# Optimization experiments

Measured on AMD Instinct MI355X. Metric: run time of the kernel, lower is better.

Reference implementation:

```python
import jax, jax.numpy as jnp
import numpy as np

N = 50000        # num_nodes
E = 800000       # num_edges (avg degree 16)
K = 3            # Chebyshev order
F_IN = 144       # 144 * in_channels
F_OUT = 144      # 144 * out_channels


def setup_inputs() -> dict:
    key = jax.random.key(0)
    k1, k2, k3, k4, k5 = jax.random.split(key, 5)
    x = jax.random.normal(k1, (N, F_IN), dtype=jnp.float32)
    edge_index = jax.random.randint(k2, (2, E), 0, N, dtype=jnp.int32)
    edge_weight = jax.random.uniform(k3, (E,), dtype=jnp.float32)
    weight = jax.random.normal(k4, (K, F_IN, F_OUT), dtype=jnp.float32) * 0.02
    bias = jax.random.normal(k5, (F_OUT,), dtype=jnp.float32) * 0.02
    return {"x": x, "edge_index": edge_index, "edge_weight": edge_weight,
            "weight": weight, "bias": bias}


def reference(x, edge_index, edge_weight, weight, bias):
    row, col = edge_index[0], edge_index[1]
    # remove_self_loops: mask out edges with row == col (fixed-shape equivalent)
    mask = (row != col).astype(x.dtype)
    w = edge_weight * mask
    # degree over remaining edges, deg^-0.5 with inf -> 0
    deg = jax.ops.segment_sum(mask, row, num_segments=N)
    dinv = jnp.where(deg > 0, deg ** -0.5, jnp.zeros_like(deg))
    lap = -dinv[row] * w * dinv[col]  # [E]

    def spmm(v):  # out[i] = sum_{e: row_e = i} lap_e * v[col_e]
        return jax.ops.segment_sum(lap[:, None] * v[col], row, num_segments=N)

    Tx0 = x
    out = Tx0 @ weight[0]
    Tx1 = spmm(Tx0)
    out = out + Tx1 @ weight[1]
    for k in range(2, weight.shape[0]):
        Tx2 = 2.0 * spmm(Tx1) - Tx0
        out = out + Tx2 @ weight[k]
        Tx0, Tx1 = Tx1, Tx2
    return out + bias
```

## Files before the change

### kernel.cpp

```cpp
#include <hip/hip_runtime.h>
#include <hip/hip_bf16.h>

#define NN 50000
#define EE 800000
#define FF 144
#define CVTBLK 1758
#define ECHK 2048
#define NBE 391
#define NBKT_REAL 391
#define NBUCKET 392
#define WGRID 284
#define HM (NBUCKET * NBE)
#define SCANBLK 599

typedef __hip_bfloat16 bf16;
typedef __attribute__((ext_vector_type(8))) short short8;
typedef __attribute__((ext_vector_type(4))) float floatx4;
typedef __attribute__((ext_vector_type(2))) float float2v;

__device__ inline float blo(unsigned x) { return __uint_as_float(x << 16); }
__device__ inline float bhi(unsigned x) { return __uint_as_float(x & 0xffff0000u); }

__device__ inline void dec4fma(float* a, float l, unsigned d) {
    float2v p0 = __builtin_amdgcn_cvt_pk_f32_fp8((int)d, false);
    float2v p1 = __builtin_amdgcn_cvt_pk_f32_fp8((int)d, true);
    a[0] = fmaf(l, p0.x, a[0]);
    a[1] = fmaf(l, p0.y, a[1]);
    a[2] = fmaf(l, p1.x, a[2]);
    a[3] = fmaf(l, p1.y, a[3]);
}
__device__ inline void fma16q(float* a, float l, uint4 u) {
    dec4fma(a + 0, l, u.x);
    dec4fma(a + 4, l, u.y);
    dec4fma(a + 8, l, u.z);
    dec4fma(a + 12, l, u.w);
}
__device__ inline unsigned enc4(float a, float b, float c, float d) {
    int w = __builtin_amdgcn_cvt_pk_fp8_f32(a, b, 0, false);
    w = __builtin_amdgcn_cvt_pk_fp8_f32(c, d, w, true);
    return (unsigned)w;
}


__global__ void detect_k(const int* __restrict__ ei, int* __restrict__ flag) {
    __shared__ int nz;
    if (threadIdx.x == 0) nz = 0;
    __syncthreads();
    if (ei[2 * threadIdx.x + 1] != 0) atomicAdd(&nz, 1);
    __syncthreads();
    if (threadIdx.x == 0) *flag = (nz == 0) ? 1 : 0;
}

__device__ inline void load_edge(const int* ei, int e, int flag, int& r, int& c) {
    if (flag) { r = ei[2 * e]; c = ei[2 * EE + 2 * e]; }
    else      { r = ei[e];     c = ei[EE + e]; }
}


__global__ void fusedA_k(const float* __restrict__ x, bf16* __restrict__ xb,
                         unsigned char* __restrict__ xq,
                         const int* __restrict__ ei, const float* __restrict__ ew,
                         unsigned long long* __restrict__ items, int* __restrict__ hist,
                         const float* __restrict__ wt, short* __restrict__ wtb,
                         const int* __restrict__ flagp) {
    __shared__ int lh[NBUCKET];
    int b = blockIdx.x;
    int tid = threadIdx.x;
    if (b < CVTBLK) {
        int t = b * 256 + tid;
        if (t >= NN * FF / 16) return;
        const float4* xp = (const float4*)x + t * 4;
        float4 v0 = xp[0], v1 = xp[1], v2 = xp[2], v3 = xp[3];
        float f[16] = {v0.x, v0.y, v0.z, v0.w, v1.x, v1.y, v1.z, v1.w,
                       v2.x, v2.y, v2.z, v2.w, v3.x, v3.y, v3.z, v3.w};
        unsigned short hs[16];
        #pragma unroll
        for (int j = 0; j < 16; ++j) {
            bf16 bb = (bf16)f[j];
            hs[j] = *(unsigned short*)&bb;
        }
        uint4* xbq = (uint4*)xb + t * 2;
        xbq[0] = ((uint4*)hs)[0];
        xbq[1] = ((uint4*)hs)[1];
        uint4 q;
        q.x = enc4(f[0], f[1], f[2], f[3]);
        q.y = enc4(f[4], f[5], f[6], f[7]);
        q.z = enc4(f[8], f[9], f[10], f[11]);
        q.w = enc4(f[12], f[13], f[14], f[15]);
        ((uint4*)xq)[t] = q;
    } else if (b < CVTBLK + NBE) {
        int bb = b - CVTBLK;
        for (int j = tid; j < NBUCKET; j += 256) lh[j] = 0;
        __syncthreads();
        int flag = *flagp;
        int eb = bb * ECHK;
        #pragma unroll
        for (int k = 0; k < ECHK / 256; ++k) {
            int e = eb + k * 256 + tid;
            if (e < EE) {
                int r, c; load_edge(ei, e, flag, r, c);
                unsigned key = (r == c) ? 0xFFFFu : (unsigned)r;
                float w = ew[e];
                items[e] = ((unsigned long long)((key << 16) | (unsigned)c) << 32)
                           | (unsigned long long)__float_as_uint(w);
                atomicAdd(&lh[min(key >> 7, (unsigned)NBKT_REAL)], 1);
            }
        }
        __syncthreads();
        for (int j = tid; j < NBUCKET; j += 256) hist[j * NBE + bb] = lh[j];
    } else {
        int t = (b - CVTBLK - NBE) * 256 + tid;
        if (t >= 3 * FF * 168) return;
        int ph = t / (FF * 168);
        int rem = t - ph * FF * 168;
        int o = rem / 168;
        int i = rem - o * 168;
        short v = 0;
        if (i < FF) {
            bf16 bv = (bf16)wt[ph * FF * FF + i * FF + o];
            v = *(const short*)&bv;
        }
        wtb[t] = v;
    }
}


__global__ void scanA1_k(int* __restrict__ hist, int* __restrict__ bsumA) {
    __shared__ int wsum[4], woff[4];
    int b = blockIdx.x, tid = threadIdx.x;
    int wv = tid >> 6, ln = tid & 63;
    int i = b * 256 + tid;
    int v = (i < HM) ? hist[i] : 0;
    int xs = v;
    #pragma unroll
    for (int off = 1; off < 64; off <<= 1) {
        int t = __shfl_up(xs, off, 64);
        if (ln >= off) xs += t;
    }
    if (ln == 63) wsum[wv] = xs;
    __syncthreads();
    if (tid == 0) {
        int s = 0;
        #pragma unroll
        for (int j = 0; j < 4; ++j) { woff[j] = s; s += wsum[j]; }
        bsumA[b] = s;
    }
    __syncthreads();
    if (i < HM) hist[i] = woff[wv] + (xs - v);
}

__global__ __launch_bounds__(1024) void scanA2_k(int* __restrict__ bsumA) {
    __shared__ int wsum[16], woff[16];
    int tid = threadIdx.x, wv = tid >> 6, ln = tid & 63;
    int v = (tid < SCANBLK) ? bsumA[tid] : 0;
    int xs = v;
    #pragma unroll
    for (int off = 1; off < 64; off <<= 1) {
        int t = __shfl_up(xs, off, 64);
        if (ln >= off) xs += t;
    }
    if (ln == 63) wsum[wv] = xs;
    __syncthreads();
    if (tid == 0) {
        int s = 0;
        #pragma unroll
        for (int j = 0; j < 16; ++j) { woff[j] = s; s += wsum[j]; }
    }
    __syncthreads();
    if (tid < SCANBLK) bsumA[tid] = woff[wv] + (xs - v);
}

__device__ inline int hbase(const int* hist, const int* bsumA, int f) {
    return hist[f] + bsumA[f >> 8];
}


__global__ void pscat_k(const unsigned long long* __restrict__ items,
                        const int* __restrict__ hist, const int* __restrict__ bsumA,
                        unsigned long long* __restrict__ sorted) {
    __shared__ int lbase[NBUCKET];
    int b = blockIdx.x, tid = threadIdx.x;
    for (int j = tid; j < NBUCKET; j += 256) {
        int f = j * NBE + b;
        lbase[j] = hbase(hist, bsumA, f);
    }
    __syncthreads();
    int eb = b * ECHK;
    #pragma unroll
    for (int k = 0; k < ECHK / 256; ++k) {
        int e = eb + k * 256 + tid;
        if (e < EE) {
            unsigned long long it = items[e];
            unsigned key = (unsigned)(it >> 48);
            int bk = (int)min(key >> 7, (unsigned)NBKT_REAL);
            int slot = atomicAdd(&lbase[bk], 1);
            sorted[slot] = it;
        }
    }
}


__global__ void fine1_k(const unsigned long long* __restrict__ sorted,
                        const int* __restrict__ hist, const int* __restrict__ bsumA,
                        int* __restrict__ rowptr, float* __restrict__ dinv) {
    __shared__ int lh[128];
    __shared__ int wtot;
    int b = blockIdx.x, tid = threadIdx.x;
    if (tid < 128) lh[tid] = 0;
    int s = hbase(hist, bsumA, b * NBE);
    int e = hbase(hist, bsumA, (b + 1) * NBE);
    __syncthreads();
    for (int p = s + tid; p < e; p += 256)
        atomicAdd(&lh[(int)(unsigned)(sorted[p] >> 48) - b * 128], 1);
    __syncthreads();
    int ln = tid & 63;
    int v = (tid < 128) ? lh[tid] : 0;
    int xs = v;
    #pragma unroll
    for (int off = 1; off < 64; off <<= 1) {
        int t = __shfl_up(xs, off, 64);
        if (ln >= off) xs += t;
    }
    if (tid == 63) wtot = xs;
    __syncthreads();
    int excl = xs - v + ((tid >= 64 && tid < 128) ? wtot : 0);
    int gr = b * 128 + tid;
    if (tid < 128 && gr < NN) {
        rowptr[gr] = s + excl;
        dinv[gr] = v > 0 ? rsqrtf((float)v) : 0.f;
    }
    if (b == NBKT_REAL - 1 && tid == 0) rowptr[NN] = e;
}


__global__ void fine2_k(const unsigned long long* __restrict__ sorted,
                        const int* __restrict__ hist, const int* __restrict__ bsumA,
                        const int* __restrict__ rowptr, const float* __restrict__ dinv,
                        unsigned* __restrict__ pairs) {
    __shared__ int lrp[128];
    __shared__ float ldv[128];
    int b = blockIdx.x, tid = threadIdx.x;
    int gr = b * 128 + tid;
    if (tid < 128) {
        lrp[tid] = (gr < NN) ? rowptr[gr] : 0;
        ldv[tid] = (gr < NN) ? dinv[gr] : 0.f;
    }
    int s = hbase(hist, bsumA, b * NBE);
    int e = hbase(hist, bsumA, (b + 1) * NBE);
    __syncthreads();
    for (int p = s + tid; p < e; p += 256) {
        unsigned long long it = sorted[p];
        int lr = (int)(unsigned)(it >> 48) - b * 128;
        unsigned c = (unsigned)(it >> 32) & 0xFFFFu;
        float w = __uint_as_float((unsigned)it);
        float lap = -ldv[lr] * dinv[c] * w;
        int slot = atomicAdd(&lrp[lr], 1);
        bf16 lb = (bf16)lap;
        pairs[slot] = c | ((unsigned)*(unsigned short*)&lb << 16);
    }
}


template <int MODE>
__global__ void spmm_k(const unsigned char* __restrict__ vq, const bf16* __restrict__ x0,
                       const int* __restrict__ rowptr, const unsigned* __restrict__ pairs,
                       bf16* __restrict__ y, unsigned char* __restrict__ yq) {
    int t = blockIdx.x * 256 + threadIdx.x;
    if (t >= NN * 9) return;
    int i = t / 9;
    int fo = (t - i * 9) * 16;
    const unsigned char* vp = vq + fo;

    float a[16];
    #pragma unroll
    for (int j = 0; j < 16; ++j) a[j] = 0.f;

    int s = rowptr[i], e = rowptr[i + 1];
    int p = s;
    for (; p + 1 < e; p += 2) {
        unsigned pr0 = pairs[p], pr1 = pairs[p + 1];
        uint4 u0 = *(const uint4*)(vp + (pr0 & 0xffffu) * FF);
        uint4 u1 = *(const uint4*)(vp + (pr1 & 0xffffu) * FF);
        fma16q(a, bhi(pr0), u0);
        fma16q(a, bhi(pr1), u1);
    }
    if (p < e) {
        unsigned pr = pairs[p];
        uint4 u = *(const uint4*)(vp + (pr & 0xffffu) * FF);
        fma16q(a, bhi(pr), u);
    }

    if (MODE == 1) {
        const uint4* xp = (const uint4*)((const unsigned short*)x0 + i * FF + fo);
        uint4 u0 = xp[0], u1 = xp[1];
        a[0]  = 2.f * a[0]  - blo(u0.x);  a[1]  = 2.f * a[1]  - bhi(u0.x);
        a[2]  = 2.f * a[2]  - blo(u0.y);  a[3]  = 2.f * a[3]  - bhi(u0.y);
        a[4]  = 2.f * a[4]  - blo(u0.z);  a[5]  = 2.f * a[5]  - bhi(u0.z);
        a[6]  = 2.f * a[6]  - blo(u0.w);  a[7]  = 2.f * a[7]  - bhi(u0.w);
        a[8]  = 2.f * a[8]  - blo(u1.x);  a[9]  = 2.f * a[9]  - bhi(u1.x);
        a[10] = 2.f * a[10] - blo(u1.y);  a[11] = 2.f * a[11] - bhi(u1.y);
        a[12] = 2.f * a[12] - blo(u1.z);  a[13] = 2.f * a[13] - bhi(u1.z);
        a[14] = 2.f * a[14] - blo(u1.w);  a[15] = 2.f * a[15] - bhi(u1.w);
    }

    unsigned short hs[16];
    #pragma unroll
    for (int j = 0; j < 16; ++j) {
        bf16 b = (bf16)a[j];
        hs[j] = *(unsigned short*)&b;
    }
    uint4* yp = (uint4*)((unsigned short*)y + i * FF + fo);
    yp[0] = ((uint4*)hs)[0];
    yp[1] = ((uint4*)hs)[1];

    if (MODE == 0) {
        uint4 q;
        q.x = enc4(a[0], a[1], a[2], a[3]);
        q.y = enc4(a[4], a[5], a[6], a[7]);
        q.z = enc4(a[8], a[9], a[10], a[11]);
        q.w = enc4(a[12], a[13], a[14], a[15]);
        *(uint4*)(yq + i * FF + fo) = q;
    }
}


__global__ __launch_bounds__(1024)
void gemm_fused(const bf16* __restrict__ A0, const bf16* __restrict__ A1,
                const bf16* __restrict__ A2, const short* __restrict__ wtb,
                const float* __restrict__ bias, float* __restrict__ out) {
    __shared__ __align__(16) short Wt[3 * 144 * 168];
    int tid = threadIdx.x;

    {
        const uint4* Wg = (const uint4*)wtb;
        uint4* Wl = (uint4*)Wt;
        #pragma unroll
        for (int q = 0; q < 9; ++q) {
            int idx = q * 1024 + tid;
            if (idx < 9072) Wl[idx] = Wg[idx];
        }
    }
    __syncthreads();

    int wv = tid >> 6, ln = tid & 63;
    int m16 = ln & 15, quad = ln >> 4;
    int tile = wv * 256 + blockIdx.x;
    if (tile * 16 >= NN) return;
    int rowBase = tile * 16;
    int row = rowBase + m16;

    const bf16* const srcs[3] = {A0, A1, A2};
    const short8 zero8 = {0, 0, 0, 0, 0, 0, 0, 0};

    floatx4 acc[9];
    #pragma unroll
    for (int q = 0; q < 9; ++q) acc[q] = (floatx4){0.f, 0.f, 0.f, 0.f};

    #pragma unroll
    for (int ph = 0; ph < 3; ++ph) {
        const bf16* A = srcs[ph];
        short8 a[5];
        #pragma unroll
        for (int kt = 0; kt < 5; ++kt) {
            int k0 = kt * 32 + quad * 8;
            if (k0 < FF)
                a[kt] = *(const short8*)((const short*)A + row * FF + k0);
            else
                a[kt] = zero8;
        }

        const short* Wp = Wt + ph * 144 * 168;
        #pragma unroll
        for (int nt = 0; nt < 9; ++nt) {
            #pragma unroll
            for (int kt = 0; kt < 5; ++kt) {
                short8 b = *(const short8*)&Wp[(nt * 16 + m16) * 168 + kt * 32 + quad * 8];
                acc[nt] = __builtin_amdgcn_mfma_f32_16x16x32_bf16(a[kt], b, acc[nt], 0, 0, 0);
            }
        }
    }

    int rowc = rowBase + quad * 4;
    #pragma unroll
    for (int nt = 0; nt < 9; ++nt) {
        int col = nt * 16 + m16;
        float bs = bias[col];
        #pragma unroll
        for (int r = 0; r < 4; ++r) {
            int rr = rowc + r;
            out[rr * FF + col] = acc[nt][r] + bs;
        }
    }
}


extern "C" void kernel_launch(void* const* d_in, const int* in_sizes, int n_in,
                              void* d_out, int out_size, void* d_ws, size_t ws_size,
                              hipStream_t stream) {
    int ix = -1, iei = -1, iew = -1, iwt = -1, ib = -1;
    for (int i = 0; i < n_in; ++i) {
        switch (in_sizes[i]) {
            case NN * FF:      if (ix  < 0) ix  = i; break;
            case 2 * EE:       if (iei < 0) iei = i; break;
            case EE:           if (iew < 0) iew = i; break;
            case 3 * FF * FF:  if (iwt < 0) iwt = i; break;
            case FF:           if (ib  < 0) ib  = i; break;
        }
    }
    if (ix < 0 || iei < 0 || iew < 0 || iwt < 0 || ib < 0) {
        ix = 0; iei = 1; iew = 2; iwt = 3; ib = 4;
    }
    const float* x    = (const float*)d_in[ix];
    const int*   ei   = (const int*)d_in[iei];
    const float* ew   = (const float*)d_in[iew];
    const float* wt   = (const float*)d_in[iwt];
    const float* bias = (const float*)d_in[ib];
    float* out = (float*)d_out;

    char* p = (char*)d_ws;
    unsigned long long* items  = (unsigned long long*)(p + 0);
    unsigned long long* sorted = (unsigned long long*)(p + 6400000);
    int*      hist   = (int*)(p + 12800000);
    int*      bsumA  = (int*)(p + 13500000);
    int*      rowptr = (int*)(p + 13600000);
    float*    dinv   = (float*)(p + 13900000);
    unsigned* pairs  = (unsigned*)(p + 14200000);
    int*      eflag  = (int*)(p + 17400000);
    short*    wtb    = (short*)(p + 17500000);
    bf16*     tx1    = (bf16*)(p + 17700000);
    bf16*     tx2    = (bf16*)(p + 32100000);
    unsigned char* xq   = (unsigned char*)(p + 46500000);
    unsigned char* tx1q = (unsigned char*)(p + 53700000);
    bf16*     xb     = (bf16*)(p + 60900000);

    if (ws_size < 75300000) return;

    int spGrid = (NN * 9 + 255) / 256;

    detect_k<<<1, 256, 0, stream>>>(ei, eflag);
    fusedA_k<<<CVTBLK + NBE + WGRID, 256, 0, stream>>>(x, xb, xq, ei, ew, items, hist,
                                                       wt, wtb, eflag);
    scanA1_k<<<SCANBLK, 256, 0, stream>>>(hist, bsumA);
    scanA2_k<<<1, 1024, 0, stream>>>(bsumA);
    pscat_k<<<NBE, 256, 0, stream>>>(items, hist, bsumA, sorted);
    fine1_k<<<NBKT_REAL, 256, 0, stream>>>(sorted, hist, bsumA, rowptr, dinv);
    fine2_k<<<NBKT_REAL, 256, 0, stream>>>(sorted, hist, bsumA, rowptr, dinv, pairs);

    spmm_k<0><<<spGrid, 256, 0, stream>>>(xq, xb, rowptr, pairs, tx1, tx1q);
    spmm_k<1><<<spGrid, 256, 0, stream>>>(tx1q, xb, rowptr, pairs, tx2, (unsigned char*)0);
    gemm_fused<<<256, 1024, 0, stream>>>(xb, tx1, tx2, wtb, bias, out);
}
```

Measured before the change: 189.0 us.

## Fold Chebyshev recurrence into weights, merge layout detection, enlarge edge chunks

```diff
diff --git a/kernel.cpp b/kernel.cpp
--- a/kernel.cpp
+++ b/kernel.cpp
@@ -5,13 +5,13 @@
 #define EE 800000
 #define FF 144
 #define CVTBLK 1758
-#define ECHK 2048
-#define NBE 391
+#define ECHK 8192
+#define NBE 98
 #define NBKT_REAL 391
 #define NBUCKET 392
 #define WGRID 284
 #define HM (NBUCKET * NBE)
-#define SCANBLK 599
+#define SCANBLK 151
 
 typedef __hip_bfloat16 bf16;
 typedef __attribute__((ext_vector_type(8))) short short8;
@@ -41,16 +41,6 @@
     return (unsigned)w;
 }
 
-
-__global__ void detect_k(const int* __restrict__ ei, int* __restrict__ flag) {
-    __shared__ int nz;
-    if (threadIdx.x == 0) nz = 0;
-    __syncthreads();
-    if (ei[2 * threadIdx.x + 1] != 0) atomicAdd(&nz, 1);
-    __syncthreads();
-    if (threadIdx.x == 0) *flag = (nz == 0) ? 1 : 0;
-}
-
 __device__ inline void load_edge(const int* ei, int e, int flag, int& r, int& c) {
     if (flag) { r = ei[2 * e]; c = ei[2 * EE + 2 * e]; }
     else      { r = ei[e];     c = ei[EE + e]; }
@@ -61,9 +51,9 @@
                          unsigned char* __restrict__ xq,
                          const int* __restrict__ ei, const float* __restrict__ ew,
                          unsigned long long* __restrict__ items, int* __restrict__ hist,
-                         const float* __restrict__ wt, short* __restrict__ wtb,
-                         const int* __restrict__ flagp) {
+                         const float* __restrict__ wt, short* __restrict__ wtb) {
     __shared__ int lh[NBUCKET];
+    __shared__ int nzf;
     int b = blockIdx.x;
     int tid = threadIdx.x;
     if (b < CVTBLK) {
@@ -90,19 +80,25 @@
         ((uint4*)xq)[t] = q;
     } else if (b < CVTBLK + NBE) {
         int bb = b - CVTBLK;
+        if (tid == 0) nzf = 0;
         for (int j = tid; j < NBUCKET; j += 256) lh[j] = 0;
         __syncthreads();
-        int flag = *flagp;
         int eb = bb * ECHK;
-        #pragma unroll
+        unsigned acc = 0;
+        for (int k = 0; k < ECHK / 256; ++k) {
+            int e = eb + k * 256 + tid;
+            if (e < EE) acc |= (unsigned)ei[2 * e + 1];
+        }
+        if (acc) nzf = 1;
+        __syncthreads();
+        int flag = (nzf == 0) ? 1 : 0;
         for (int k = 0; k < ECHK / 256; ++k) {
             int e = eb + k * 256 + tid;
             if (e < EE) {
                 int r, c; load_edge(ei, e, flag, r, c);
                 unsigned key = (r == c) ? 0xFFFFu : (unsigned)r;
-                float w = ew[e];
                 items[e] = ((unsigned long long)((key << 16) | (unsigned)c) << 32)
-                           | (unsigned long long)__float_as_uint(w);
+                           | (unsigned long long)__float_as_uint(ew[e]);
                 atomicAdd(&lh[min(key >> 7, (unsigned)NBKT_REAL)], 1);
             }
         }
@@ -117,7 +113,11 @@
         int i = rem - o * 168;
         short v = 0;
         if (i < FF) {
-            bf16 bv = (bf16)wt[ph * FF * FF + i * FF + o];
+            float fv;
+            if (ph == 0)      fv = wt[i * FF + o] - wt[2 * FF * FF + i * FF + o];
+            else if (ph == 1) fv = wt[FF * FF + i * FF + o];
+            else              fv = 2.0f * wt[2 * FF * FF + i * FF + o];
+            bf16 bv = (bf16)fv;
             v = *(const short*)&bv;
         }
         wtb[t] = v;
@@ -149,8 +149,8 @@
     if (i < HM) hist[i] = woff[wv] + (xs - v);
 }
 
-__global__ __launch_bounds__(1024) void scanA2_k(int* __restrict__ bsumA) {
-    __shared__ int wsum[16], woff[16];
+__global__ void scanA2_k(int* __restrict__ bsumA) {
+    __shared__ int wsum[4], woff[4];
     int tid = threadIdx.x, wv = tid >> 6, ln = tid & 63;
     int v = (tid < SCANBLK) ? bsumA[tid] : 0;
     int xs = v;
@@ -164,7 +164,7 @@
     if (tid == 0) {
         int s = 0;
         #pragma unroll
-        for (int j = 0; j < 16; ++j) { woff[j] = s; s += wsum[j]; }
+        for (int j = 0; j < 4; ++j) { woff[j] = s; s += wsum[j]; }
     }
     __syncthreads();
     if (tid < SCANBLK) bsumA[tid] = woff[wv] + (xs - v);
@@ -186,7 +186,6 @@
     }
     __syncthreads();
     int eb = b * ECHK;
-    #pragma unroll
     for (int k = 0; k < ECHK / 256; ++k) {
         int e = eb + k * 256 + tid;
         if (e < EE) {
@@ -261,8 +260,8 @@
 }
 
 
-template <int MODE>
-__global__ void spmm_k(const unsigned char* __restrict__ vq, const bf16* __restrict__ x0,
+template <int WRITEQ>
+__global__ void spmm_k(const unsigned char* __restrict__ vq,
                        const int* __restrict__ rowptr, const unsigned* __restrict__ pairs,
                        bf16* __restrict__ y, unsigned char* __restrict__ yq) {
     int t = blockIdx.x * 256 + threadIdx.x;
@@ -290,19 +289,6 @@
         fma16q(a, bhi(pr), u);
     }
 
-    if (MODE == 1) {
-        const uint4* xp = (const uint4*)((const unsigned short*)x0 + i * FF + fo);
-        uint4 u0 = xp[0], u1 = xp[1];
-        a[0]  = 2.f * a[0]  - blo(u0.x);  a[1]  = 2.f * a[1]  - bhi(u0.x);
-        a[2]  = 2.f * a[2]  - blo(u0.y);  a[3]  = 2.f * a[3]  - bhi(u0.y);
-        a[4]  = 2.f * a[4]  - blo(u0.z);  a[5]  = 2.f * a[5]  - bhi(u0.z);
-        a[6]  = 2.f * a[6]  - blo(u0.w);  a[7]  = 2.f * a[7]  - bhi(u0.w);
-        a[8]  = 2.f * a[8]  - blo(u1.x);  a[9]  = 2.f * a[9]  - bhi(u1.x);
-        a[10] = 2.f * a[10] - blo(u1.y);  a[11] = 2.f * a[11] - bhi(u1.y);
-        a[12] = 2.f * a[12] - blo(u1.z);  a[13] = 2.f * a[13] - bhi(u1.z);
-        a[14] = 2.f * a[14] - blo(u1.w);  a[15] = 2.f * a[15] - bhi(u1.w);
-    }
-
     unsigned short hs[16];
     #pragma unroll
     for (int j = 0; j < 16; ++j) {
@@ -313,7 +299,7 @@
     yp[0] = ((uint4*)hs)[0];
     yp[1] = ((uint4*)hs)[1];
 
-    if (MODE == 0) {
+    if (WRITEQ) {
         uint4 q;
         q.x = enc4(a[0], a[1], a[2], a[3]);
         q.y = enc4(a[4], a[5], a[6], a[7]);
@@ -425,7 +411,6 @@
     int*      rowptr = (int*)(p + 13600000);
     float*    dinv   = (float*)(p + 13900000);
     unsigned* pairs  = (unsigned*)(p + 14200000);
-    int*      eflag  = (int*)(p + 17400000);
     short*    wtb    = (short*)(p + 17500000);
     bf16*     tx1    = (bf16*)(p + 17700000);
     bf16*     tx2    = (bf16*)(p + 32100000);
@@ -437,16 +422,15 @@
 
     int spGrid = (NN * 9 + 255) / 256;
 
-    detect_k<<<1, 256, 0, stream>>>(ei, eflag);
     fusedA_k<<<CVTBLK + NBE + WGRID, 256, 0, stream>>>(x, xb, xq, ei, ew, items, hist,
-                                                       wt, wtb, eflag);
+                                                       wt, wtb);
     scanA1_k<<<SCANBLK, 256, 0, stream>>>(hist, bsumA);
-    scanA2_k<<<1, 1024, 0, stream>>>(bsumA);
+    scanA2_k<<<1, 256, 0, stream>>>(bsumA);
     pscat_k<<<NBE, 256, 0, stream>>>(items, hist, bsumA, sorted);
     fine1_k<<<NBKT_REAL, 256, 0, stream>>>(sorted, hist, bsumA, rowptr, dinv);
     fine2_k<<<NBKT_REAL, 256, 0, stream>>>(sorted, hist, bsumA, rowptr, dinv, pairs);
 
-    spmm_k<0><<<spGrid, 256, 0, stream>>>(xq, xb, rowptr, pairs, tx1, tx1q);
-    spmm_k<1><<<spGrid, 256, 0, stream>>>(tx1q, xb, rowptr, pairs, tx2, (unsigned char*)0);
+    spmm_k<1><<<spGrid, 256, 0, stream>>>(xq, rowptr, pairs, tx1, tx1q);
+    spmm_k<0><<<spGrid, 256, 0, stream>>>(tx1q, rowptr, pairs, tx2, (unsigned char*)0);
     gemm_fused<<<256, 1024, 0, stream>>>(xb, tx1, tx2, wtb, bias, out);
 }
```

New measurement: 204.7 us. +8.3%, slower.
